# Performance work log

Measured on AMD Instinct MI355X. Metric: run time of the kernel, lower is better.

The kernel has to match this reference:

```python
import jax, jax.numpy as jnp
from jax import lax
import numpy as np

B, T, I, H, C = 2048, 512, 46, 64, 8

def setup_inputs() -> dict:
    key = jax.random.key(0)
    ks = jax.random.split(key, 7)
    s_ih = 1.0 / np.sqrt(H)  # PyTorch GRU init scale ~ U(-1/sqrt(H), 1/sqrt(H)); use scaled normal
    return {
        "x": jax.random.normal(ks[0], (B, T, I), jnp.float32),
        "w_ih": jax.random.normal(ks[1], (3 * H, I), jnp.float32) * s_ih,
        "w_hh": jax.random.normal(ks[2], (3 * H, H), jnp.float32) * s_ih,
        "b_ih": jax.random.normal(ks[3], (3 * H,), jnp.float32) * s_ih,
        "b_hh": jax.random.normal(ks[4], (3 * H,), jnp.float32) * s_ih,
        "fc_w": jax.random.normal(ks[5], (C, H), jnp.float32) * (1.0 / np.sqrt(H)),
        "fc_b": jax.random.normal(ks[6], (C,), jnp.float32) * (1.0 / np.sqrt(H)),
    }

def reference(x, w_ih, w_hh, b_ih, b_hh, fc_w, fc_b):
    # x: [B, T, I]. PyTorch GRU gate order: r, z, n.
    Bv, Tv, _ = x.shape
    Hv = w_hh.shape[1]
    # Precompute input contributions for all timesteps: [B, T, 3H]
    gx = jnp.einsum('bti,gi->btg', x, w_ih) + b_ih
    gx_t = jnp.swapaxes(gx, 0, 1)  # [T, B, 3H] for scan

    def step(h, gxt):
        gh = h @ w_hh.T + b_hh  # [B, 3H]
        xr, xz, xn = jnp.split(gxt, 3, axis=-1)
        hr, hz, hn = jnp.split(gh, 3, axis=-1)
        r = jax.nn.sigmoid(xr + hr)
        z = jax.nn.sigmoid(xz + hz)
        n = jnp.tanh(xn + r * hn)
        h_new = (1.0 - z) * n + z * h
        return h_new, None

    h0 = jnp.zeros((Bv, Hv), x.dtype)
    h_last, _ = lax.scan(step, h0, gx_t)  # last hidden == output[:, -1, :]
    logits = h_last @ fc_w.T + fc_b  # [B, C]
    return jax.nn.softmax(logits, axis=1)
```

## Files before the change

kernel.cpp:

```cpp
#include <hip/hip_runtime.h>
#include <hip/hip_bf16.h>

#define TT 512
#define II 46
#define HH 64
#define GG 192
#define CC 8
#define RR 8
#define KP 128

typedef __attribute__((ext_vector_type(8))) _Float16 half8;
typedef __attribute__((ext_vector_type(4))) float float4v;

__device__ inline float fsigm(float xv) {
  return __builtin_amdgcn_rcpf(1.f + __expf(-xv));
}
__device__ inline float ftanh2(float xv) {
  float e = __expf(2.f * xv);
  return __builtin_fmaf(-2.f, __builtin_amdgcn_rcpf(1.f + e), 1.f);
}

__device__ inline void barrier_lds_only() {
  asm volatile("s_waitcnt lgkmcnt(0)" ::: "memory");
  __builtin_amdgcn_s_barrier();
  asm volatile("" ::: "memory");
}

__global__ void pack_w(const float* __restrict__ w_ih, const float* __restrict__ w_hh,
                       _Float16* __restrict__ wp) {
  int idx = blockIdx.x * 256 + threadIdx.x;
  int u = idx >> 7, k = idx & 127;
  float v = (k < HH) ? w_hh[u * HH + k]
                     : ((k < HH + II) ? w_ih[u * II + (k - HH)] : 0.f);
  wp[idx] = (_Float16)v;
}

__launch_bounds__(256, 1)
__global__ void gru_main(const float* __restrict__ x,
                         const float* __restrict__ b_ih, const float* __restrict__ b_hh,
                         const float* __restrict__ fc_w, const float* __restrict__ fc_b,
                         const _Float16* __restrict__ wp,
                         float* __restrict__ out) {
  __shared__ __align__(16) _Float16 hsf[2][2][64][8];
  __shared__ __align__(16) _Float16 xsf[4][2][64][8];
  __shared__ float hf[RR][HH + 1];
  __shared__ float fcw[CC * HH];
  __shared__ float fcbs[CC];
  __shared__ float lgts[RR][CC];

  const int tau = threadIdx.x;
  const int w4  = tau >> 6;
  const int l   = tau & 63;
  const int m16 = l & 15;
  const int kg  = l >> 4;
  const int row0 = blockIdx.x * RR;

  {
    _Float16* p = &hsf[0][0][0][0];
    for (int i = tau; i < 2 * 2 * 64 * 8; i += 256) p[i] = (_Float16)0.f;
    p = &xsf[0][0][0][0];
    for (int i = tau; i < 4 * 2 * 64 * 8; i += 256) p[i] = (_Float16)0.f;
  }

  const int u = 16 * w4 + m16;
  const float br  = b_ih[u] + b_hh[u];
  const float bz  = b_ih[64 + u] + b_hh[64 + u];
  const float bnx = b_ih[128 + u];
  const float bnh = b_hh[128 + u];

  half8 bhr[2], bhz[2], bhn[2], bxr[2], bxz[2], bxn[2];
  {
    const _Float16* rr = wp + (size_t)u * KP + 8 * kg;
    const _Float16* rz = wp + (size_t)(64 + u) * KP + 8 * kg;
    const _Float16* rn = wp + (size_t)(128 + u) * KP + 8 * kg;
    bhr[0] = *(const half8*)(rr);      bhr[1] = *(const half8*)(rr + 32);
    bxr[0] = *(const half8*)(rr + 64); bxr[1] = *(const half8*)(rr + 96);
    bhz[0] = *(const half8*)(rz);      bhz[1] = *(const half8*)(rz + 32);
    bxz[0] = *(const half8*)(rz + 64); bxz[1] = *(const half8*)(rz + 96);
    bhn[0] = *(const half8*)(rn);      bhn[1] = *(const half8*)(rn + 32);
    bxn[0] = *(const half8*)(rn + 64); bxn[1] = *(const half8*)(rn + 96);
  }

  const int sh  = w4 >> 1;
  const int kgp = (u >> 3) & 3;
  const int jp  = u & 7;

  const int r1 = tau / II, i1 = tau % II;
  const int m1 = (r1 >> 1) * 4 + (r1 & 1);
  const bool has2 = (tau + 256) < RR * II;
  const int e2 = tau + 256;
  const int r2 = has2 ? e2 / II : r1, i2 = has2 ? e2 % II : i1;
  const int m2 = (r2 >> 1) * 4 + (r2 & 1);
  const float* xp1 = x + (size_t)(row0 + r1) * TT * II + i1;
  const float* xp2 = x + (size_t)(row0 + r2) * TT * II + i2;
  const int s1 = i1 >> 5, kg1 = (i1 >> 3) & 3, j1 = i1 & 7;
  const int s2 = i2 >> 5, kg2 = (i2 >> 3) & 3, j2 = i2 & 7;

  auto stageX = [&](int buf, float va, float vb) {
    xsf[buf][s1][kg1 * 16 + m1][j1] = (_Float16)va;
    if (has2) xsf[buf][s2][kg2 * 16 + m2][j2] = (_Float16)vb;
  };

  float hreg[2] = {0.f, 0.f};

  float v0a = xp1[0],            v0b = has2 ? xp2[0] : 0.f;
  float v1a = xp1[II],           v1b = has2 ? xp2[II] : 0.f;
  float xc1 = xp1[2 * II],       xc2 = has2 ? xp2[2 * II] : 0.f;
  float xn1 = xp1[3 * II],       xn2 = has2 ? xp2[3 * II] : 0.f;
  __syncthreads();
  stageX(0, v0a, v0b);
  stageX(1, v1a, v1b);
  __syncthreads();

  float4v xrA = {br, br, br, br};
  float4v xzA = {bz, bz, bz, bz};
  float4v xnA = {bnx, bnx, bnx, bnx};
  {
    half8 c0 = *(const half8*)&xsf[0][0][l][0];
    half8 c1 = *(const half8*)&xsf[0][1][l][0];
    xrA = __builtin_amdgcn_mfma_f32_16x16x32_f16(c0, bxr[0], xrA, 0, 0, 0);
    xzA = __builtin_amdgcn_mfma_f32_16x16x32_f16(c0, bxz[0], xzA, 0, 0, 0);
    xnA = __builtin_amdgcn_mfma_f32_16x16x32_f16(c0, bxn[0], xnA, 0, 0, 0);
    xrA = __builtin_amdgcn_mfma_f32_16x16x32_f16(c1, bxr[1], xrA, 0, 0, 0);
    xzA = __builtin_amdgcn_mfma_f32_16x16x32_f16(c1, bxz[1], xzA, 0, 0, 0);
    xnA = __builtin_amdgcn_mfma_f32_16x16x32_f16(c1, bxn[1], xnA, 0, 0, 0);
  }
  float4v xrB, xzB, xnB;

  auto iter = [&](int t, int cur, int nb, int sb,
                  float4v& xrC, float4v& xzC, float4v& xnC,
                  float4v& xrN, float4v& xzN, float4v& xnN) {
    barrier_lds_only();
    const int nxt = cur ^ 1;
    half8 a0 = *(const half8*)&hsf[cur][0][l][0];
    half8 a1 = *(const half8*)&hsf[cur][1][l][0];
    half8 c0 = *(const half8*)&xsf[nb][0][l][0];
    half8 c1 = *(const half8*)&xsf[nb][1][l][0];

    float4v nh4 = {bnh, bnh, bnh, bnh};
    float4v accr  = __builtin_amdgcn_mfma_f32_16x16x32_f16(a0, bhr[0], xrC, 0, 0, 0);
    float4v accz  = __builtin_amdgcn_mfma_f32_16x16x32_f16(a0, bhz[0], xzC, 0, 0, 0);
    float4v accnh = __builtin_amdgcn_mfma_f32_16x16x32_f16(a0, bhn[0], nh4, 0, 0, 0);
    accr  = __builtin_amdgcn_mfma_f32_16x16x32_f16(a1, bhr[1], accr, 0, 0, 0);
    accz  = __builtin_amdgcn_mfma_f32_16x16x32_f16(a1, bhz[1], accz, 0, 0, 0);
    accnh = __builtin_amdgcn_mfma_f32_16x16x32_f16(a1, bhn[1], accnh, 0, 0, 0);

    xrN = (float4v){br, br, br, br};
    xzN = (float4v){bz, bz, bz, bz};
    xnN = (float4v){bnx, bnx, bnx, bnx};
    xrN = __builtin_amdgcn_mfma_f32_16x16x32_f16(c0, bxr[0], xrN, 0, 0, 0);
    xzN = __builtin_amdgcn_mfma_f32_16x16x32_f16(c0, bxz[0], xzN, 0, 0, 0);
    xnN = __builtin_amdgcn_mfma_f32_16x16x32_f16(c0, bxn[0], xnN, 0, 0, 0);
    xrN = __builtin_amdgcn_mfma_f32_16x16x32_f16(c1, bxr[1], xrN, 0, 0, 0);
    xzN = __builtin_amdgcn_mfma_f32_16x16x32_f16(c1, bxz[1], xzN, 0, 0, 0);
    xnN = __builtin_amdgcn_mfma_f32_16x16x32_f16(c1, bxn[1], xnN, 0, 0, 0);

#pragma unroll
    for (int i = 0; i < 2; ++i) {
      float rg = fsigm(accr[i]);
      float zg = fsigm(accz[i]);
      float pre = __builtin_fmaf(rg, accnh[i], xnC[i]);
      float ng = ftanh2(pre);
      hreg[i] = __builtin_fmaf(zg, hreg[i] - ng, ng);
      hsf[nxt][sh][kgp * 16 + kg * 4 + i][jp] = (_Float16)hreg[i];
    }

    stageX(sb, xc1, xc2);
    xc1 = xn1; xc2 = xn2;
    if (t + 4 < TT) {
      xn1 = xp1[(size_t)(t + 4) * II];
      if (has2) xn2 = xp2[(size_t)(t + 4) * II];
    }
  };

  for (int t = 0; t < TT; t += 4) {
    iter(t,     0, 1, 2, xrA, xzA, xnA, xrB, xzB, xnB);
    iter(t + 1, 1, 2, 3, xrB, xzB, xnB, xrA, xzA, xnA);
    iter(t + 2, 0, 3, 0, xrA, xzA, xnA, xrB, xzB, xnB);
    iter(t + 3, 1, 0, 1, xrB, xzB, xnB, xrA, xzA, xnA);
  }

  hf[2 * kg + 0][u] = hreg[0];
  hf[2 * kg + 1][u] = hreg[1];
  fcw[tau] = fc_w[tau];
  fcw[tau + 256] = fc_w[tau + 256];
  if (tau < CC) fcbs[tau] = fc_b[tau];
  __syncthreads();
  if (tau < RR * CC) {
    int rr = tau >> 3, c = tau & 7;
    float acc = fcbs[c];
#pragma unroll
    for (int j = 0; j < HH; ++j) acc += hf[rr][j] * fcw[c * HH + j];
    lgts[rr][c] = acc;
  }
  __syncthreads();
  if (tau < RR * CC) {
    int rr = tau >> 3, c = tau & 7;
    float mx = lgts[rr][0];
#pragma unroll
    for (int j = 1; j < CC; ++j) mx = fmaxf(mx, lgts[rr][j]);
    float ssum = 0.f;
#pragma unroll
    for (int j = 0; j < CC; ++j) ssum += __expf(lgts[rr][j] - mx);
    out[(size_t)(row0 + rr) * CC + c] = __expf(lgts[rr][c] - mx) / ssum;
  }
}

extern "C" void kernel_launch(void* const* d_in, const int* in_sizes, int n_in,
                              void* d_out, int out_size, void* d_ws, size_t ws_size,
                              hipStream_t stream) {
  const float* x    = (const float*)d_in[0];
  const float* w_ih = (const float*)d_in[1];
  const float* w_hh = (const float*)d_in[2];
  const float* b_ih = (const float*)d_in[3];
  const float* b_hh = (const float*)d_in[4];
  const float* fc_w = (const float*)d_in[5];
  const float* fc_b = (const float*)d_in[6];

  _Float16* wp = (_Float16*)d_ws;

  pack_w<<<96, 256, 0, stream>>>(w_ih, w_hh, wp);
  gru_main<<<256, 256, 0, stream>>>(x, b_ih, b_hh, fc_w, fc_b, wp, (float*)d_out);
}
```

Baseline: 191.1 us.

## Load x directly into MFMA fragment registers, removing LDS staging

Each lane now loads its own x elements as float2 pairs straight from global memory into registers, packs them to fp16 with cvt_pkrtz, and feeds them to the input-projection MFMAs. This replaces the scalar global loads, the LDS x staging buffers and the LDS fragment reads. The goal is to cut LDS traffic and per-step latency on the serial recurrence. In exchange it needs more registers for the prefetch buffers (two timesteps ahead) and issues more global loads per lane. Half the lanes are predicated off via bval.

After: 319.0 us. 1.67x slower.

```diff
diff --git a/kernel.cpp b/kernel.cpp
--- a/kernel.cpp
+++ b/kernel.cpp
@@ -10,7 +10,10 @@
 #define KP 128
 
 typedef __attribute__((ext_vector_type(8))) _Float16 half8;
+typedef __attribute__((ext_vector_type(2))) _Float16 half2v;
+typedef __attribute__((ext_vector_type(2))) __fp16 fp16x2;
 typedef __attribute__((ext_vector_type(4))) float float4v;
+typedef __attribute__((ext_vector_type(2))) float float2v;
 
 __device__ inline float fsigm(float xv) {
   return __builtin_amdgcn_rcpf(1.f + __expf(-xv));
@@ -42,7 +45,6 @@
                          const _Float16* __restrict__ wp,
                          float* __restrict__ out) {
   __shared__ __align__(16) _Float16 hsf[2][2][64][8];
-  __shared__ __align__(16) _Float16 xsf[4][2][64][8];
   __shared__ float hf[RR][HH + 1];
   __shared__ float fcw[CC * HH];
   __shared__ float fcbs[CC];
@@ -58,8 +60,6 @@
   {
     _Float16* p = &hsf[0][0][0][0];
     for (int i = tau; i < 2 * 2 * 64 * 8; i += 256) p[i] = (_Float16)0.f;
-    p = &xsf[0][0][0][0];
-    for (int i = tau; i < 4 * 2 * 64 * 8; i += 256) p[i] = (_Float16)0.f;
   }
 
   const int u = 16 * w4 + m16;
@@ -85,57 +85,74 @@
   const int kgp = (u >> 3) & 3;
   const int jp  = u & 7;
 
-  const int r1 = tau / II, i1 = tau % II;
-  const int m1 = (r1 >> 1) * 4 + (r1 & 1);
-  const bool has2 = (tau + 256) < RR * II;
-  const int e2 = tau + 256;
-  const int r2 = has2 ? e2 / II : r1, i2 = has2 ? e2 % II : i1;
-  const int m2 = (r2 >> 1) * 4 + (r2 & 1);
-  const float* xp1 = x + (size_t)(row0 + r1) * TT * II + i1;
-  const float* xp2 = x + (size_t)(row0 + r2) * TT * II + i2;
-  const int s1 = i1 >> 5, kg1 = (i1 >> 3) & 3, j1 = i1 & 7;
-  const int s2 = i2 >> 5, kg2 = (i2 >> 3) & 3, j2 = i2 & 7;
-
-  auto stageX = [&](int buf, float va, float vb) {
-    xsf[buf][s1][kg1 * 16 + m1][j1] = (_Float16)va;
-    if (has2) xsf[buf][s2][kg2 * 16 + m2][j2] = (_Float16)vb;
+  const int  brow = 2 * (m16 >> 2) + (m16 & 1);
+  const bool bval = ((m16 & 3) < 2);
+  const float* xr_ = x + (size_t)(row0 + brow) * TT * II;
+
+  float2v P[8], Q[8], T0[8], T1[8];
+#pragma unroll
+  for (int j = 0; j < 8; ++j) {
+    P[j] = (float2v){0.f, 0.f}; Q[j] = (float2v){0.f, 0.f};
+    T0[j] = (float2v){0.f, 0.f}; T1[j] = (float2v){0.f, 0.f};
+  }
+
+  auto loadX = [&](int tt, float2v* p) {
+    if (bval && tt < TT) {
+      const float* base = xr_ + (size_t)tt * II;
+#pragma unroll
+      for (int j = 0; j < 4; ++j) {
+        int d = 8 * kg + 2 * j;
+        p[j] = *(const float2v*)(base + d);
+      }
+#pragma unroll
+      for (int j = 0; j < 4; ++j) {
+        int d = 32 + 8 * kg + 2 * j;
+        if (d + 1 < II) p[4 + j] = *(const float2v*)(base + d);
+      }
+    }
+  };
+  auto cvt2 = [](float a, float b) -> half2v {
+    fp16x2 q = __builtin_amdgcn_cvt_pkrtz(a, b);
+    return __builtin_bit_cast(half2v, q);
+  };
+  auto mkfrag = [&](const float2v* p) -> half8 {
+    half2v q0 = cvt2(p[0][0], p[0][1]);
+    half2v q1 = cvt2(p[1][0], p[1][1]);
+    half2v q2 = cvt2(p[2][0], p[2][1]);
+    half2v q3 = cvt2(p[3][0], p[3][1]);
+    half8 c = {q0[0], q0[1], q1[0], q1[1], q2[0], q2[1], q3[0], q3[1]};
+    return c;
   };
 
   float hreg[2] = {0.f, 0.f};
 
-  float v0a = xp1[0],            v0b = has2 ? xp2[0] : 0.f;
-  float v1a = xp1[II],           v1b = has2 ? xp2[II] : 0.f;
-  float xc1 = xp1[2 * II],       xc2 = has2 ? xp2[2 * II] : 0.f;
-  float xn1 = xp1[3 * II],       xn2 = has2 ? xp2[3 * II] : 0.f;
   __syncthreads();
-  stageX(0, v0a, v0b);
-  stageX(1, v1a, v1b);
-  __syncthreads();
-
-  float4v xrA = {br, br, br, br};
-  float4v xzA = {bz, bz, bz, bz};
-  float4v xnA = {bnx, bnx, bnx, bnx};
-  {
-    half8 c0 = *(const half8*)&xsf[0][0][l][0];
-    half8 c1 = *(const half8*)&xsf[0][1][l][0];
-    xrA = __builtin_amdgcn_mfma_f32_16x16x32_f16(c0, bxr[0], xrA, 0, 0, 0);
-    xzA = __builtin_amdgcn_mfma_f32_16x16x32_f16(c0, bxz[0], xzA, 0, 0, 0);
-    xnA = __builtin_amdgcn_mfma_f32_16x16x32_f16(c0, bxn[0], xnA, 0, 0, 0);
-    xrA = __builtin_amdgcn_mfma_f32_16x16x32_f16(c1, bxr[1], xrA, 0, 0, 0);
-    xzA = __builtin_amdgcn_mfma_f32_16x16x32_f16(c1, bxz[1], xzA, 0, 0, 0);
-    xnA = __builtin_amdgcn_mfma_f32_16x16x32_f16(c1, bxn[1], xnA, 0, 0, 0);
-  }
+
+  loadX(0, T0);
+  loadX(1, T1);
+  half8 g0 = mkfrag(T0), g1 = mkfrag(T0 + 4);
+  half8 fC0 = mkfrag(T1), fC1 = mkfrag(T1 + 4);
+  half8 fD0 = fC0, fD1 = fC1;
+  float4v xrA = {br, br, br, br}, xzA = {bz, bz, bz, bz}, xnA = {bnx, bnx, bnx, bnx};
+  xrA = __builtin_amdgcn_mfma_f32_16x16x32_f16(g0, bxr[0], xrA, 0, 0, 0);
+  xzA = __builtin_amdgcn_mfma_f32_16x16x32_f16(g0, bxz[0], xzA, 0, 0, 0);
+  xnA = __builtin_amdgcn_mfma_f32_16x16x32_f16(g0, bxn[0], xnA, 0, 0, 0);
+  xrA = __builtin_amdgcn_mfma_f32_16x16x32_f16(g1, bxr[1], xrA, 0, 0, 0);
+  xzA = __builtin_amdgcn_mfma_f32_16x16x32_f16(g1, bxz[1], xzA, 0, 0, 0);
+  xnA = __builtin_amdgcn_mfma_f32_16x16x32_f16(g1, bxn[1], xnA, 0, 0, 0);
   float4v xrB, xzB, xnB;
-
-  auto iter = [&](int t, int cur, int nb, int sb,
+  loadX(2, P);
+  loadX(3, Q);
+
+  auto iter = [&](int t, int cur,
                   float4v& xrC, float4v& xzC, float4v& xnC,
-                  float4v& xrN, float4v& xzN, float4v& xnN) {
+                  float4v& xrN, float4v& xzN, float4v& xnN,
+                  half8& fu0, half8& fu1, half8& fm0, half8& fm1,
+                  float2v* pend) {
     barrier_lds_only();
     const int nxt = cur ^ 1;
     half8 a0 = *(const half8*)&hsf[cur][0][l][0];
     half8 a1 = *(const half8*)&hsf[cur][1][l][0];
-    half8 c0 = *(const half8*)&xsf[nb][0][l][0];
-    half8 c1 = *(const half8*)&xsf[nb][1][l][0];
 
     float4v nh4 = {bnh, bnh, bnh, bnh};
     float4v accr  = __builtin_amdgcn_mfma_f32_16x16x32_f16(a0, bhr[0], xrC, 0, 0, 0);
@@ -148,12 +165,16 @@
     xrN = (float4v){br, br, br, br};
     xzN = (float4v){bz, bz, bz, bz};
     xnN = (float4v){bnx, bnx, bnx, bnx};
-    xrN = __builtin_amdgcn_mfma_f32_16x16x32_f16(c0, bxr[0], xrN, 0, 0, 0);
-    xzN = __builtin_amdgcn_mfma_f32_16x16x32_f16(c0, bxz[0], xzN, 0, 0, 0);
-    xnN = __builtin_amdgcn_mfma_f32_16x16x32_f16(c0, bxn[0], xnN, 0, 0, 0);
-    xrN = __builtin_amdgcn_mfma_f32_16x16x32_f16(c1, bxr[1], xrN, 0, 0, 0);
-    xzN = __builtin_amdgcn_mfma_f32_16x16x32_f16(c1, bxz[1], xzN, 0, 0, 0);
-    xnN = __builtin_amdgcn_mfma_f32_16x16x32_f16(c1, bxn[1], xnN, 0, 0, 0);
+    xrN = __builtin_amdgcn_mfma_f32_16x16x32_f16(fu0, bxr[0], xrN, 0, 0, 0);
+    xzN = __builtin_amdgcn_mfma_f32_16x16x32_f16(fu0, bxz[0], xzN, 0, 0, 0);
+    xnN = __builtin_amdgcn_mfma_f32_16x16x32_f16(fu0, bxn[0], xnN, 0, 0, 0);
+    xrN = __builtin_amdgcn_mfma_f32_16x16x32_f16(fu1, bxr[1], xrN, 0, 0, 0);
+    xzN = __builtin_amdgcn_mfma_f32_16x16x32_f16(fu1, bxz[1], xzN, 0, 0, 0);
+    xnN = __builtin_amdgcn_mfma_f32_16x16x32_f16(fu1, bxn[1], xnN, 0, 0, 0);
+
+    fm0 = mkfrag(pend);
+    fm1 = mkfrag(pend + 4);
+    loadX(t + 4, pend);
 
 #pragma unroll
     for (int i = 0; i < 2; ++i) {
@@ -164,20 +185,11 @@
       hreg[i] = __builtin_fmaf(zg, hreg[i] - ng, ng);
       hsf[nxt][sh][kgp * 16 + kg * 4 + i][jp] = (_Float16)hreg[i];
     }
-
-    stageX(sb, xc1, xc2);
-    xc1 = xn1; xc2 = xn2;
-    if (t + 4 < TT) {
-      xn1 = xp1[(size_t)(t + 4) * II];
-      if (has2) xn2 = xp2[(size_t)(t + 4) * II];
-    }
-  };
-
-  for (int t = 0; t < TT; t += 4) {
-    iter(t,     0, 1, 2, xrA, xzA, xnA, xrB, xzB, xnB);
-    iter(t + 1, 1, 2, 3, xrB, xzB, xnB, xrA, xzA, xnA);
-    iter(t + 2, 0, 3, 0, xrA, xzA, xnA, xrB, xzB, xnB);
-    iter(t + 3, 1, 0, 1, xrB, xzB, xnB, xrA, xzA, xnA);
+  };
+
+  for (int t = 0; t < TT; t += 2) {
+    iter(t,     0, xrA, xzA, xnA, xrB, xzB, xnB, fC0, fC1, fD0, fD1, P);
+    iter(t + 1, 1, xrB, xzB, xnB, xrA, xzA, xnA, fD0, fD1, fC0, fC1, Q);
   }
 
   hf[2 * kg + 0][u] = hreg[0];
```

## Pack two timesteps per MFMA for input projection, halving x-projection MFMAs

Applied to the files above, without the earlier changes.

The kernel now places two consecutive timesteps' inputs into the unused accumulator rows of each 16-row MFMA tile. Rows 2 and 3 of each group of four hold timestep t+1, so one set of six input-projection MFMAs covers two recurrent steps. The second step's gate inputs are taken from those extra accumulator lanes via shuffles. The x staging buffer shrinks to two slots and the prefetch schedule is rewritten to load three elements per thread every two steps. This removes half of the input-side MFMA work on the serial critical path, at the cost of more complex staging and barriers between the paired steps.

New measurement: 274.3 us. +43.5%, slower.

```diff
diff --git a/kernel.cpp b/kernel.cpp
--- a/kernel.cpp
+++ b/kernel.cpp
@@ -42,7 +42,7 @@
                          const _Float16* __restrict__ wp,
                          float* __restrict__ out) {
   __shared__ __align__(16) _Float16 hsf[2][2][64][8];
-  __shared__ __align__(16) _Float16 xsf[4][2][64][8];
+  __shared__ __align__(16) _Float16 xsf[2][2][64][8];
   __shared__ float hf[RR][HH + 1];
   __shared__ float fcw[CC * HH];
   __shared__ float fcbs[CC];
@@ -59,8 +59,9 @@
     _Float16* p = &hsf[0][0][0][0];
     for (int i = tau; i < 2 * 2 * 64 * 8; i += 256) p[i] = (_Float16)0.f;
     p = &xsf[0][0][0][0];
-    for (int i = tau; i < 4 * 2 * 64 * 8; i += 256) p[i] = (_Float16)0.f;
-  }
+    for (int i = tau; i < 2 * 2 * 64 * 8; i += 256) p[i] = (_Float16)0.f;
+  }
+  __syncthreads();
 
   const int u = 16 * w4 + m16;
   const float br  = b_ih[u] + b_hh[u];
@@ -85,99 +86,132 @@
   const int kgp = (u >> 3) & 3;
   const int jp  = u & 7;
 
-  const int r1 = tau / II, i1 = tau % II;
-  const int m1 = (r1 >> 1) * 4 + (r1 & 1);
-  const bool has2 = (tau + 256) < RR * II;
-  const int e2 = tau + 256;
-  const int r2 = has2 ? e2 / II : r1, i2 = has2 ? e2 % II : i1;
-  const int m2 = (r2 >> 1) * 4 + (r2 & 1);
-  const float* xp1 = x + (size_t)(row0 + r1) * TT * II + i1;
-  const float* xp2 = x + (size_t)(row0 + r2) * TT * II + i2;
-  const int s1 = i1 >> 5, kg1 = (i1 >> 3) & 3, j1 = i1 & 7;
-  const int s2 = i2 >> 5, kg2 = (i2 >> 3) & 3, j2 = i2 & 7;
-
-  auto stageX = [&](int buf, float va, float vb) {
-    xsf[buf][s1][kg1 * 16 + m1][j1] = (_Float16)va;
-    if (has2) xsf[buf][s2][kg2 * 16 + m2][j2] = (_Float16)vb;
+  bool ev_[3]; int es_[3], eln[3], ej_[3];
+  const float* ep_[3];
+#pragma unroll
+  for (int q = 0; q < 3; ++q) {
+    int e = tau + 256 * q;
+    ev_[q] = e < 2 * RR * II;
+    int e2 = ev_[q] ? e : 0;
+    int sg = (e2 >= RR * II) ? 1 : 0;
+    int rem = e2 - RR * II * sg;
+    int b = rem / II, i = rem % II;
+    es_[q] = i >> 5;
+    eln[q] = ((i >> 3) & 3) * 16 + (b >> 1) * 4 + (b & 1) + 2 * sg;
+    ej_[q] = i & 7;
+    ep_[q] = x + (size_t)(row0 + b) * TT * II + (size_t)sg * II + i;
+  }
+
+  float hreg[2] = {0.f, 0.f};
+
+  float pA[3], pB[3];
+  {
+    float pd0[3], pd1[3];
+#pragma unroll
+    for (int q = 0; q < 3; ++q) {
+      pd0[q] = ev_[q] ? ep_[q][0] : 0.f;
+      pd1[q] = ev_[q] ? ep_[q][2 * II] : 0.f;
+      pA[q]  = ev_[q] ? ep_[q][4 * II] : 0.f;
+    }
+#pragma unroll
+    for (int q = 0; q < 3; ++q) if (ev_[q]) xsf[0][es_[q]][eln[q]][ej_[q]] = (_Float16)pd0[q];
+#pragma unroll
+    for (int q = 0; q < 3; ++q) if (ev_[q]) xsf[1][es_[q]][eln[q]][ej_[q]] = (_Float16)pd1[q];
+  }
+  __syncthreads();
+
+  auto xm = [&](const half8& c0, const half8& c1,
+                float4v& xr, float4v& xz, float4v& xn) {
+    xr = (float4v){br, br, br, br};
+    xz = (float4v){bz, bz, bz, bz};
+    xn = (float4v){bnx, bnx, bnx, bnx};
+    xr = __builtin_amdgcn_mfma_f32_16x16x32_f16(c0, bxr[0], xr, 0, 0, 0);
+    xz = __builtin_amdgcn_mfma_f32_16x16x32_f16(c0, bxz[0], xz, 0, 0, 0);
+    xn = __builtin_amdgcn_mfma_f32_16x16x32_f16(c0, bxn[0], xn, 0, 0, 0);
+    xr = __builtin_amdgcn_mfma_f32_16x16x32_f16(c1, bxr[1], xr, 0, 0, 0);
+    xz = __builtin_amdgcn_mfma_f32_16x16x32_f16(c1, bxz[1], xz, 0, 0, 0);
+    xn = __builtin_amdgcn_mfma_f32_16x16x32_f16(c1, bxn[1], xn, 0, 0, 0);
   };
 
-  float hreg[2] = {0.f, 0.f};
-
-  float v0a = xp1[0],            v0b = has2 ? xp2[0] : 0.f;
-  float v1a = xp1[II],           v1b = has2 ? xp2[II] : 0.f;
-  float xc1 = xp1[2 * II],       xc2 = has2 ? xp2[2 * II] : 0.f;
-  float xn1 = xp1[3 * II],       xn2 = has2 ? xp2[3 * II] : 0.f;
-  __syncthreads();
-  stageX(0, v0a, v0b);
-  stageX(1, v1a, v1b);
-  __syncthreads();
-
-  float4v xrA = {br, br, br, br};
-  float4v xzA = {bz, bz, bz, bz};
-  float4v xnA = {bnx, bnx, bnx, bnx};
+  float4v xrA, xzA, xnA, xrB, xzB, xnB;
   {
     half8 c0 = *(const half8*)&xsf[0][0][l][0];
     half8 c1 = *(const half8*)&xsf[0][1][l][0];
-    xrA = __builtin_amdgcn_mfma_f32_16x16x32_f16(c0, bxr[0], xrA, 0, 0, 0);
-    xzA = __builtin_amdgcn_mfma_f32_16x16x32_f16(c0, bxz[0], xzA, 0, 0, 0);
-    xnA = __builtin_amdgcn_mfma_f32_16x16x32_f16(c0, bxn[0], xnA, 0, 0, 0);
-    xrA = __builtin_amdgcn_mfma_f32_16x16x32_f16(c1, bxr[1], xrA, 0, 0, 0);
-    xzA = __builtin_amdgcn_mfma_f32_16x16x32_f16(c1, bxz[1], xzA, 0, 0, 0);
-    xnA = __builtin_amdgcn_mfma_f32_16x16x32_f16(c1, bxn[1], xnA, 0, 0, 0);
-  }
-  float4v xrB, xzB, xnB;
-
-  auto iter = [&](int t, int cur, int nb, int sb,
-                  float4v& xrC, float4v& xzC, float4v& xnC,
-                  float4v& xrN, float4v& xzN, float4v& xnN) {
-    barrier_lds_only();
-    const int nxt = cur ^ 1;
+    xm(c0, c1, xrA, xzA, xnA);
+  }
+
+  const float* pp0 = ep_[0] + 6 * II;
+  const float* pp1 = ep_[1] + 6 * II;
+  const float* pp2 = ep_[2] + 6 * II;
+
+  auto hcore = [&](int cur, float4v cr, float4v cz, float xn0, float xn1) {
     half8 a0 = *(const half8*)&hsf[cur][0][l][0];
     half8 a1 = *(const half8*)&hsf[cur][1][l][0];
-    half8 c0 = *(const half8*)&xsf[nb][0][l][0];
-    half8 c1 = *(const half8*)&xsf[nb][1][l][0];
-
     float4v nh4 = {bnh, bnh, bnh, bnh};
-    float4v accr  = __builtin_amdgcn_mfma_f32_16x16x32_f16(a0, bhr[0], xrC, 0, 0, 0);
-    float4v accz  = __builtin_amdgcn_mfma_f32_16x16x32_f16(a0, bhz[0], xzC, 0, 0, 0);
-    float4v accnh = __builtin_amdgcn_mfma_f32_16x16x32_f16(a0, bhn[0], nh4, 0, 0, 0);
-    accr  = __builtin_amdgcn_mfma_f32_16x16x32_f16(a1, bhr[1], accr, 0, 0, 0);
-    accz  = __builtin_amdgcn_mfma_f32_16x16x32_f16(a1, bhz[1], accz, 0, 0, 0);
-    accnh = __builtin_amdgcn_mfma_f32_16x16x32_f16(a1, bhn[1], accnh, 0, 0, 0);
-
-    xrN = (float4v){br, br, br, br};
-    xzN = (float4v){bz, bz, bz, bz};
-    xnN = (float4v){bnx, bnx, bnx, bnx};
-    xrN = __builtin_amdgcn_mfma_f32_16x16x32_f16(c0, bxr[0], xrN, 0, 0, 0);
-    xzN = __builtin_amdgcn_mfma_f32_16x16x32_f16(c0, bxz[0], xzN, 0, 0, 0);
-    xnN = __builtin_amdgcn_mfma_f32_16x16x32_f16(c0, bxn[0], xnN, 0, 0, 0);
-    xrN = __builtin_amdgcn_mfma_f32_16x16x32_f16(c1, bxr[1], xrN, 0, 0, 0);
-    xzN = __builtin_amdgcn_mfma_f32_16x16x32_f16(c1, bxz[1], xzN, 0, 0, 0);
-    xnN = __builtin_amdgcn_mfma_f32_16x16x32_f16(c1, bxn[1], xnN, 0, 0, 0);
-
-#pragma unroll
-    for (int i = 0; i < 2; ++i) {
-      float rg = fsigm(accr[i]);
-      float zg = fsigm(accz[i]);
-      float pre = __builtin_fmaf(rg, accnh[i], xnC[i]);
-      float ng = ftanh2(pre);
-      hreg[i] = __builtin_fmaf(zg, hreg[i] - ng, ng);
-      hsf[nxt][sh][kgp * 16 + kg * 4 + i][jp] = (_Float16)hreg[i];
-    }
-
-    stageX(sb, xc1, xc2);
-    xc1 = xn1; xc2 = xn2;
-    if (t + 4 < TT) {
-      xn1 = xp1[(size_t)(t + 4) * II];
-      if (has2) xn2 = xp2[(size_t)(t + 4) * II];
-    }
+    float4v ar = __builtin_amdgcn_mfma_f32_16x16x32_f16(a0, bhr[0], cr, 0, 0, 0);
+    float4v az = __builtin_amdgcn_mfma_f32_16x16x32_f16(a0, bhz[0], cz, 0, 0, 0);
+    float4v an = __builtin_amdgcn_mfma_f32_16x16x32_f16(a0, bhn[0], nh4, 0, 0, 0);
+    ar = __builtin_amdgcn_mfma_f32_16x16x32_f16(a1, bhr[1], ar, 0, 0, 0);
+    az = __builtin_amdgcn_mfma_f32_16x16x32_f16(a1, bhz[1], az, 0, 0, 0);
+    an = __builtin_amdgcn_mfma_f32_16x16x32_f16(a1, bhn[1], an, 0, 0, 0);
+    const int nxt = cur ^ 1;
+    float rg0 = fsigm(ar[0]), zg0 = fsigm(az[0]);
+    float rg1 = fsigm(ar[1]), zg1 = fsigm(az[1]);
+    float ng0 = ftanh2(__builtin_fmaf(rg0, an[0], xn0));
+    float ng1 = ftanh2(__builtin_fmaf(rg1, an[1], xn1));
+    hreg[0] = __builtin_fmaf(zg0, hreg[0] - ng0, ng0);
+    hreg[1] = __builtin_fmaf(zg1, hreg[1] - ng1, ng1);
+    hsf[nxt][sh][kgp * 16 + kg * 4 + 0][jp] = (_Float16)hreg[0];
+    hsf[nxt][sh][kgp * 16 + kg * 4 + 1][jp] = (_Float16)hreg[1];
   };
 
-  for (int t = 0; t < TT; t += 4) {
-    iter(t,     0, 1, 2, xrA, xzA, xnA, xrB, xzB, xnB);
-    iter(t + 1, 1, 2, 3, xrB, xzB, xnB, xrA, xzA, xnA);
-    iter(t + 2, 0, 3, 0, xrA, xzA, xnA, xrB, xzB, xnB);
-    iter(t + 3, 1, 0, 1, xrB, xzB, xnB, xrA, xzA, xnA);
+  for (int q = 0; q < TT / 4; ++q) {
+    const int j0 = 2 * q;
+    barrier_lds_only();
+#pragma unroll
+    for (int s3 = 0; s3 < 3; ++s3)
+      if (ev_[s3]) xsf[0][es_[s3]][eln[s3]][ej_[s3]] = (_Float16)pA[s3];
+    {
+      const bool ok = (j0 + 3) < TT / 2;
+      pB[0] = (ev_[0] && ok) ? pp0[0] : 0.f;
+      pB[1] = (ev_[1] && ok) ? pp1[0] : 0.f;
+      pB[2] = (ev_[2] && ok) ? pp2[0] : 0.f;
+      pp0 += 2 * II; pp1 += 2 * II; pp2 += 2 * II;
+    }
+    hcore(0, xrA, xzA, xnA[0], xnA[1]);
+
+    barrier_lds_only();
+    {
+      half8 c0 = *(const half8*)&xsf[1][0][l][0];
+      half8 c1 = *(const half8*)&xsf[1][1][l][0];
+      float4v cr = __builtin_shufflevector(xrA, xrA, 2, 3, 2, 3);
+      float4v cz = __builtin_shufflevector(xzA, xzA, 2, 3, 2, 3);
+      hcore(1, cr, cz, xnA[2], xnA[3]);
+      xm(c0, c1, xrB, xzB, xnB);
+    }
+
+    barrier_lds_only();
+#pragma unroll
+    for (int s3 = 0; s3 < 3; ++s3)
+      if (ev_[s3]) xsf[1][es_[s3]][eln[s3]][ej_[s3]] = (_Float16)pB[s3];
+    {
+      const bool ok = (j0 + 4) < TT / 2;
+      pA[0] = (ev_[0] && ok) ? pp0[0] : 0.f;
+      pA[1] = (ev_[1] && ok) ? pp1[0] : 0.f;
+      pA[2] = (ev_[2] && ok) ? pp2[0] : 0.f;
+      pp0 += 2 * II; pp1 += 2 * II; pp2 += 2 * II;
+    }
+    hcore(0, xrB, xzB, xnB[0], xnB[1]);
+
+    barrier_lds_only();
+    {
+      half8 c0 = *(const half8*)&xsf[0][0][l][0];
+      half8 c1 = *(const half8*)&xsf[0][1][l][0];
+      float4v cr = __builtin_shufflevector(xrB, xrB, 2, 3, 2, 3);
+      float4v cz = __builtin_shufflevector(xzB, xzB, 2, 3, 2, 3);
+      hcore(1, cr, cz, xnB[2], xnB[3]);
+      xm(c0, c1, xrA, xzA, xnA);
+    }
   }
 
   hf[2 * kg + 0][u] = hreg[0];
```

## Split GRU block into consumer waves for recurrence and producer waves for input projection

Applied to the files above, without the earlier changes.

Doubles the block to 512 threads. Four waves run only the recurrent h@W_hh MFMAs and gate math. Four producer waves compute the input projection for the next step, stage x, and pass the gate pre-activations through a double-buffered LDS array, taking that work off the serial critical path. It also folds the factor of 2 inside tanh into the packed n-gate weights and biases to drop one multiply. The cost is an extra LDS round-trip per step, and barrier counts across the two roles must line up exactly (three empty syncthreads are added on the consumer side).

Result: faster. 176.1 us, median of 2 (-7.9%).

```diff
diff --git a/kernel.cpp b/kernel.cpp
--- a/kernel.cpp
+++ b/kernel.cpp
@@ -8,6 +8,7 @@
 #define CC 8
 #define RR 8
 #define KP 128
+#define GXPAD 10
 
 typedef __attribute__((ext_vector_type(8))) _Float16 half8;
 typedef __attribute__((ext_vector_type(4))) float float4v;
@@ -15,8 +16,8 @@
 __device__ inline float fsigm(float xv) {
   return __builtin_amdgcn_rcpf(1.f + __expf(-xv));
 }
-__device__ inline float ftanh2(float xv) {
-  float e = __expf(2.f * xv);
+__device__ inline float ftanh_pre2(float pre2) {
+  float e = __expf(pre2);
   return __builtin_fmaf(-2.f, __builtin_amdgcn_rcpf(1.f + e), 1.f);
 }
 
@@ -32,10 +33,11 @@
   int u = idx >> 7, k = idx & 127;
   float v = (k < HH) ? w_hh[u * HH + k]
                      : ((k < HH + II) ? w_ih[u * II + (k - HH)] : 0.f);
+  if (u >= 128) v *= 2.f;
   wp[idx] = (_Float16)v;
 }
 
-__launch_bounds__(256, 1)
+__launch_bounds__(512, 2)
 __global__ void gru_main(const float* __restrict__ x,
                          const float* __restrict__ b_ih, const float* __restrict__ b_hh,
                          const float* __restrict__ fc_w, const float* __restrict__ fc_b,
@@ -43,13 +45,14 @@
                          float* __restrict__ out) {
   __shared__ __align__(16) _Float16 hsf[2][2][64][8];
   __shared__ __align__(16) _Float16 xsf[4][2][64][8];
+  __shared__ __align__(16) float gxpT[2][3][64][GXPAD];
   __shared__ float hf[RR][HH + 1];
   __shared__ float fcw[CC * HH];
   __shared__ float fcbs[CC];
   __shared__ float lgts[RR][CC];
 
   const int tau = threadIdx.x;
-  const int w4  = tau >> 6;
+  const int w8  = tau >> 6;
   const int l   = tau & 63;
   const int m16 = l & 15;
   const int kg  = l >> 4;
@@ -57,133 +60,164 @@
 
   {
     _Float16* p = &hsf[0][0][0][0];
-    for (int i = tau; i < 2 * 2 * 64 * 8; i += 256) p[i] = (_Float16)0.f;
+    for (int i = tau; i < 2 * 2 * 64 * 8; i += 512) p[i] = (_Float16)0.f;
     p = &xsf[0][0][0][0];
-    for (int i = tau; i < 4 * 2 * 64 * 8; i += 256) p[i] = (_Float16)0.f;
-  }
-
-  const int u = 16 * w4 + m16;
-  const float br  = b_ih[u] + b_hh[u];
-  const float bz  = b_ih[64 + u] + b_hh[64 + u];
-  const float bnx = b_ih[128 + u];
-  const float bnh = b_hh[128 + u];
-
-  half8 bhr[2], bhz[2], bhn[2], bxr[2], bxz[2], bxn[2];
-  {
-    const _Float16* rr = wp + (size_t)u * KP + 8 * kg;
-    const _Float16* rz = wp + (size_t)(64 + u) * KP + 8 * kg;
-    const _Float16* rn = wp + (size_t)(128 + u) * KP + 8 * kg;
-    bhr[0] = *(const half8*)(rr);      bhr[1] = *(const half8*)(rr + 32);
-    bxr[0] = *(const half8*)(rr + 64); bxr[1] = *(const half8*)(rr + 96);
-    bhz[0] = *(const half8*)(rz);      bhz[1] = *(const half8*)(rz + 32);
-    bxz[0] = *(const half8*)(rz + 64); bxz[1] = *(const half8*)(rz + 96);
-    bhn[0] = *(const half8*)(rn);      bhn[1] = *(const half8*)(rn + 32);
-    bxn[0] = *(const half8*)(rn + 64); bxn[1] = *(const half8*)(rn + 96);
-  }
-
-  const int sh  = w4 >> 1;
-  const int kgp = (u >> 3) & 3;
-  const int jp  = u & 7;
-
-  const int r1 = tau / II, i1 = tau % II;
-  const int m1 = (r1 >> 1) * 4 + (r1 & 1);
-  const bool has2 = (tau + 256) < RR * II;
-  const int e2 = tau + 256;
-  const int r2 = has2 ? e2 / II : r1, i2 = has2 ? e2 % II : i1;
-  const int m2 = (r2 >> 1) * 4 + (r2 & 1);
-  const float* xp1 = x + (size_t)(row0 + r1) * TT * II + i1;
-  const float* xp2 = x + (size_t)(row0 + r2) * TT * II + i2;
-  const int s1 = i1 >> 5, kg1 = (i1 >> 3) & 3, j1 = i1 & 7;
-  const int s2 = i2 >> 5, kg2 = (i2 >> 3) & 3, j2 = i2 & 7;
-
-  auto stageX = [&](int buf, float va, float vb) {
-    xsf[buf][s1][kg1 * 16 + m1][j1] = (_Float16)va;
-    if (has2) xsf[buf][s2][kg2 * 16 + m2][j2] = (_Float16)vb;
-  };
+    for (int i = tau; i < 4 * 2 * 64 * 8; i += 512) p[i] = (_Float16)0.f;
+  }
 
   float hreg[2] = {0.f, 0.f};
 
-  float v0a = xp1[0],            v0b = has2 ? xp2[0] : 0.f;
-  float v1a = xp1[II],           v1b = has2 ? xp2[II] : 0.f;
-  float xc1 = xp1[2 * II],       xc2 = has2 ? xp2[2 * II] : 0.f;
-  float xn1 = xp1[3 * II],       xn2 = has2 ? xp2[3 * II] : 0.f;
-  __syncthreads();
-  stageX(0, v0a, v0b);
-  stageX(1, v1a, v1b);
-  __syncthreads();
-
-  float4v xrA = {br, br, br, br};
-  float4v xzA = {bz, bz, bz, bz};
-  float4v xnA = {bnx, bnx, bnx, bnx};
-  {
-    half8 c0 = *(const half8*)&xsf[0][0][l][0];
-    half8 c1 = *(const half8*)&xsf[0][1][l][0];
-    xrA = __builtin_amdgcn_mfma_f32_16x16x32_f16(c0, bxr[0], xrA, 0, 0, 0);
-    xzA = __builtin_amdgcn_mfma_f32_16x16x32_f16(c0, bxz[0], xzA, 0, 0, 0);
-    xnA = __builtin_amdgcn_mfma_f32_16x16x32_f16(c0, bxn[0], xnA, 0, 0, 0);
-    xrA = __builtin_amdgcn_mfma_f32_16x16x32_f16(c1, bxr[1], xrA, 0, 0, 0);
-    xzA = __builtin_amdgcn_mfma_f32_16x16x32_f16(c1, bxz[1], xzA, 0, 0, 0);
-    xnA = __builtin_amdgcn_mfma_f32_16x16x32_f16(c1, bxn[1], xnA, 0, 0, 0);
-  }
-  float4v xrB, xzB, xnB;
-
-  auto iter = [&](int t, int cur, int nb, int sb,
-                  float4v& xrC, float4v& xzC, float4v& xnC,
-                  float4v& xrN, float4v& xzN, float4v& xnN) {
-    barrier_lds_only();
-    const int nxt = cur ^ 1;
-    half8 a0 = *(const half8*)&hsf[cur][0][l][0];
-    half8 a1 = *(const half8*)&hsf[cur][1][l][0];
-    half8 c0 = *(const half8*)&xsf[nb][0][l][0];
-    half8 c1 = *(const half8*)&xsf[nb][1][l][0];
-
-    float4v nh4 = {bnh, bnh, bnh, bnh};
-    float4v accr  = __builtin_amdgcn_mfma_f32_16x16x32_f16(a0, bhr[0], xrC, 0, 0, 0);
-    float4v accz  = __builtin_amdgcn_mfma_f32_16x16x32_f16(a0, bhz[0], xzC, 0, 0, 0);
-    float4v accnh = __builtin_amdgcn_mfma_f32_16x16x32_f16(a0, bhn[0], nh4, 0, 0, 0);
-    accr  = __builtin_amdgcn_mfma_f32_16x16x32_f16(a1, bhr[1], accr, 0, 0, 0);
-    accz  = __builtin_amdgcn_mfma_f32_16x16x32_f16(a1, bhz[1], accz, 0, 0, 0);
-    accnh = __builtin_amdgcn_mfma_f32_16x16x32_f16(a1, bhn[1], accnh, 0, 0, 0);
-
-    xrN = (float4v){br, br, br, br};
-    xzN = (float4v){bz, bz, bz, bz};
-    xnN = (float4v){bnx, bnx, bnx, bnx};
-    xrN = __builtin_amdgcn_mfma_f32_16x16x32_f16(c0, bxr[0], xrN, 0, 0, 0);
-    xzN = __builtin_amdgcn_mfma_f32_16x16x32_f16(c0, bxz[0], xzN, 0, 0, 0);
-    xnN = __builtin_amdgcn_mfma_f32_16x16x32_f16(c0, bxn[0], xnN, 0, 0, 0);
-    xrN = __builtin_amdgcn_mfma_f32_16x16x32_f16(c1, bxr[1], xrN, 0, 0, 0);
-    xzN = __builtin_amdgcn_mfma_f32_16x16x32_f16(c1, bxz[1], xzN, 0, 0, 0);
-    xnN = __builtin_amdgcn_mfma_f32_16x16x32_f16(c1, bxn[1], xnN, 0, 0, 0);
-
-#pragma unroll
-    for (int i = 0; i < 2; ++i) {
-      float rg = fsigm(accr[i]);
-      float zg = fsigm(accz[i]);
-      float pre = __builtin_fmaf(rg, accnh[i], xnC[i]);
-      float ng = ftanh2(pre);
-      hreg[i] = __builtin_fmaf(zg, hreg[i] - ng, ng);
-      hsf[nxt][sh][kgp * 16 + kg * 4 + i][jp] = (_Float16)hreg[i];
-    }
-
-    stageX(sb, xc1, xc2);
-    xc1 = xn1; xc2 = xn2;
-    if (t + 4 < TT) {
-      xn1 = xp1[(size_t)(t + 4) * II];
-      if (has2) xn2 = xp2[(size_t)(t + 4) * II];
-    }
-  };
-
-  for (int t = 0; t < TT; t += 4) {
-    iter(t,     0, 1, 2, xrA, xzA, xnA, xrB, xzB, xnB);
-    iter(t + 1, 1, 2, 3, xrB, xzB, xnB, xrA, xzA, xnA);
-    iter(t + 2, 0, 3, 0, xrA, xzA, xnA, xrB, xzB, xnB);
-    iter(t + 3, 1, 0, 1, xrB, xzB, xnB, xrA, xzA, xnA);
-  }
-
-  hf[2 * kg + 0][u] = hreg[0];
-  hf[2 * kg + 1][u] = hreg[1];
+  if (w8 < 4) {
+    const int u = 16 * w8 + m16;
+    const float bnh2 = 2.f * b_hh[128 + u];
+    half8 bhr[2], bhz[2], bhn[2];
+    {
+      const _Float16* rr = wp + (size_t)u * KP + 8 * kg;
+      const _Float16* rz = wp + (size_t)(64 + u) * KP + 8 * kg;
+      const _Float16* rn = wp + (size_t)(128 + u) * KP + 8 * kg;
+      bhr[0] = *(const half8*)(rr); bhr[1] = *(const half8*)(rr + 32);
+      bhz[0] = *(const half8*)(rz); bhz[1] = *(const half8*)(rz + 32);
+      bhn[0] = *(const half8*)(rn); bhn[1] = *(const half8*)(rn + 32);
+    }
+    const int sh  = w8 >> 1;
+    const int kgp = (u >> 3) & 3;
+    const int jp  = u & 7;
+
+    __syncthreads();
+    __syncthreads();
+    __syncthreads();
+
+    auto cstep = [&](int cur) {
+      barrier_lds_only();
+      const int nxt = cur ^ 1;
+      half8 a0 = *(const half8*)&hsf[cur][0][l][0];
+      half8 a1 = *(const half8*)&hsf[cur][1][l][0];
+      float2 gR = *(const float2*)&gxpT[cur][0][u][2 * kg];
+      float2 gZ = *(const float2*)&gxpT[cur][1][u][2 * kg];
+      float2 gN = *(const float2*)&gxpT[cur][2][u][2 * kg];
+
+      float4v cr = {gR.x, gR.y, gR.x, gR.y};
+      float4v cz = {gZ.x, gZ.y, gZ.x, gZ.y};
+      float4v nh4 = {bnh2, bnh2, bnh2, bnh2};
+      float4v ar = __builtin_amdgcn_mfma_f32_16x16x32_f16(a0, bhr[0], cr, 0, 0, 0);
+      float4v az = __builtin_amdgcn_mfma_f32_16x16x32_f16(a0, bhz[0], cz, 0, 0, 0);
+      float4v an = __builtin_amdgcn_mfma_f32_16x16x32_f16(a0, bhn[0], nh4, 0, 0, 0);
+      ar = __builtin_amdgcn_mfma_f32_16x16x32_f16(a1, bhr[1], ar, 0, 0, 0);
+      az = __builtin_amdgcn_mfma_f32_16x16x32_f16(a1, bhz[1], az, 0, 0, 0);
+      an = __builtin_amdgcn_mfma_f32_16x16x32_f16(a1, bhn[1], an, 0, 0, 0);
+
+      const float gn2[2] = {gN.x, gN.y};
+#pragma unroll
+      for (int i = 0; i < 2; ++i) {
+        float rg = fsigm(ar[i]);
+        float zg = fsigm(az[i]);
+        float ng = ftanh_pre2(__builtin_fmaf(rg, an[i], gn2[i]));
+        hreg[i] = __builtin_fmaf(zg, hreg[i] - ng, ng);
+        hsf[nxt][sh][kgp * 16 + kg * 4 + i][jp] = (_Float16)hreg[i];
+      }
+    };
+
+    for (int t = 0; t < TT; t += 2) {
+      cstep(0);
+      cstep(1);
+    }
+  } else {
+    const int u = 16 * (w8 - 4) + m16;
+    const float br   = b_ih[u] + b_hh[u];
+    const float bz   = b_ih[64 + u] + b_hh[64 + u];
+    const float bnx2 = 2.f * b_ih[128 + u];
+    half8 bxr[2], bxz[2], bxn[2];
+    {
+      const _Float16* rr = wp + (size_t)u * KP + 8 * kg;
+      const _Float16* rz = wp + (size_t)(64 + u) * KP + 8 * kg;
+      const _Float16* rn = wp + (size_t)(128 + u) * KP + 8 * kg;
+      bxr[0] = *(const half8*)(rr + 64); bxr[1] = *(const half8*)(rr + 96);
+      bxz[0] = *(const half8*)(rz + 64); bxz[1] = *(const half8*)(rz + 96);
+      bxn[0] = *(const half8*)(rn + 64); bxn[1] = *(const half8*)(rn + 96);
+    }
+
+    const int p = tau - 256;
+    bool ev_[2]; int es_[2], eln_[2], ej_[2];
+    const float* ep_[2];
+#pragma unroll
+    for (int q = 0; q < 2; ++q) {
+      int e = p + 256 * q;
+      ev_[q] = e < RR * II;
+      int e2 = ev_[q] ? e : 0;
+      int b = e2 / II, i = e2 % II;
+      es_[q] = i >> 5;
+      eln_[q] = ((i >> 3) & 3) * 16 + (b >> 1) * 4 + (b & 1);
+      ej_[q] = i & 7;
+      ep_[q] = x + (size_t)(row0 + b) * TT * II + i;
+    }
+
+    float v0_[2], v1_[2], xc_[2], xn_[2];
+#pragma unroll
+    for (int q = 0; q < 2; ++q) {
+      v0_[q] = ev_[q] ? ep_[q][0] : 0.f;
+      v1_[q] = ev_[q] ? ep_[q][II] : 0.f;
+      xc_[q] = ev_[q] ? ep_[q][2 * II] : 0.f;
+      xn_[q] = ev_[q] ? ep_[q][3 * II] : 0.f;
+    }
+
+    __syncthreads();
+#pragma unroll
+    for (int q = 0; q < 2; ++q) if (ev_[q]) xsf[0][es_[q]][eln_[q]][ej_[q]] = (_Float16)v0_[q];
+#pragma unroll
+    for (int q = 0; q < 2; ++q) if (ev_[q]) xsf[1][es_[q]][eln_[q]][ej_[q]] = (_Float16)v1_[q];
+    __syncthreads();
+
+    auto produce = [&](int dst, int src) {
+      half8 c0 = *(const half8*)&xsf[src][0][l][0];
+      half8 c1 = *(const half8*)&xsf[src][1][l][0];
+      float4v r4 = {br, br, br, br};
+      float4v z4 = {bz, bz, bz, bz};
+      float4v n4 = {bnx2, bnx2, bnx2, bnx2};
+      r4 = __builtin_amdgcn_mfma_f32_16x16x32_f16(c0, bxr[0], r4, 0, 0, 0);
+      z4 = __builtin_amdgcn_mfma_f32_16x16x32_f16(c0, bxz[0], z4, 0, 0, 0);
+      n4 = __builtin_amdgcn_mfma_f32_16x16x32_f16(c0, bxn[0], n4, 0, 0, 0);
+      r4 = __builtin_amdgcn_mfma_f32_16x16x32_f16(c1, bxr[1], r4, 0, 0, 0);
+      z4 = __builtin_amdgcn_mfma_f32_16x16x32_f16(c1, bxz[1], z4, 0, 0, 0);
+      n4 = __builtin_amdgcn_mfma_f32_16x16x32_f16(c1, bxn[1], n4, 0, 0, 0);
+      *(float2*)&gxpT[dst][0][u][2 * kg] = make_float2(r4[0], r4[1]);
+      *(float2*)&gxpT[dst][1][u][2 * kg] = make_float2(z4[0], z4[1]);
+      *(float2*)&gxpT[dst][2][u][2 * kg] = make_float2(n4[0], n4[1]);
+    };
+
+    produce(0, 0);
+    __syncthreads();
+
+    auto pstep = [&](int t, int nxt, int nb, int sb) {
+      barrier_lds_only();
+      if (t + 1 < TT) produce(nxt, nb);
+      if (t + 2 < TT) {
+#pragma unroll
+        for (int q = 0; q < 2; ++q)
+          if (ev_[q]) xsf[sb][es_[q]][eln_[q]][ej_[q]] = (_Float16)xc_[q];
+      }
+#pragma unroll
+      for (int q = 0; q < 2; ++q) xc_[q] = xn_[q];
+      if (t + 4 < TT) {
+#pragma unroll
+        for (int q = 0; q < 2; ++q)
+          if (ev_[q]) xn_[q] = ep_[q][(size_t)(t + 4) * II];
+      }
+    };
+
+    for (int t = 0; t < TT; t += 4) {
+      pstep(t,     1, 1, 2);
+      pstep(t + 1, 0, 2, 3);
+      pstep(t + 2, 1, 3, 0);
+      pstep(t + 3, 0, 0, 1);
+    }
+  }
+
+  if (w8 < 4) {
+    const int u = 16 * w8 + m16;
+    hf[2 * kg + 0][u] = hreg[0];
+    hf[2 * kg + 1][u] = hreg[1];
+  }
   fcw[tau] = fc_w[tau];
-  fcw[tau + 256] = fc_w[tau + 256];
   if (tau < CC) fcbs[tau] = fc_b[tau];
   __syncthreads();
   if (tau < RR * CC) {
@@ -220,5 +254,5 @@
   _Float16* wp = (_Float16*)d_ws;
 
   pack_w<<<96, 256, 0, stream>>>(w_ih, w_hh, wp);
-  gru_main<<<256, 256, 0, stream>>>(x, b_ih, b_hh, fc_w, fc_b, wp, (float*)d_out);
-}
+  gru_main<<<256, 512, 0, stream>>>(x, b_ih, b_hh, fc_w, fc_b, wp, (float*)d_out);
+}
```
